# Kernel optimization log

Measured on AMD Instinct MI355X. Metric: run time of the kernel, lower is better.

Reference implementation:

```python
import jax, jax.numpy as jnp
import numpy as np


def _closest_dist_sum(p1, p2):
    # p1: [B, N, 3], p2: [B, M, 3]
    # Euclidean distance via the expanded quadratic form; matches
    # torch.norm(p1 - p2, 2, dim=3) -> min over p2 -> sum over all.
    d2 = (jnp.sum(p1 * p1, axis=-1)[:, :, None]
          + jnp.sum(p2 * p2, axis=-1)[:, None, :]
          - 2.0 * jnp.einsum('bnd,bmd->bnm', p1, p2))  # [B, N, M]
    d = jnp.sqrt(jnp.maximum(d2, 0.0))
    return jnp.sum(jnp.min(d, axis=2))


def setup_inputs() -> dict:
    key = jax.random.key(0)
    k1, k2 = jax.random.split(key)
    shape_xyz = jax.random.normal(k1, (8, 8192, 6), dtype=jnp.float32)
    skel_xyz = jax.random.normal(k2, (8, 2048, 3), dtype=jnp.float32)
    return {"shape_xyz": shape_xyz, "skel_xyz": skel_xyz}


def reference(shape_xyz, skel_xyz):
    # normals (shape_xyz[:, :, 3:6]) are extracted but unused in the loss
    pts = shape_xyz[:, :, :3]
    cd1 = _closest_dist_sum(pts, skel_xyz)   # shape -> skeleton
    cd2 = _closest_dist_sum(skel_xyz, pts)   # skeleton -> shape
    loss_cd = (cd1 + cd2) * 0.0001
    return loss_cd
```

## Files before the change

kernel.cpp:

```cpp
#include <hip/hip_runtime.h>

#define BATCH   8
#define SHAPE_N 8192
#define SKEL_M  2048
#define CHUNK   1024

#define WS2_OFF 512

typedef short bf16x8 __attribute__((ext_vector_type(8)));
typedef float f32x16 __attribute__((ext_vector_type(16)));
union FragU { bf16x8 v; uint4 u4; };

__device__ __forceinline__ unsigned int f2bf(float a) {
    unsigned int u = __float_as_uint(a);
    return (u + 0x7FFFu + ((u >> 16) & 1u)) >> 16;
}
__device__ __forceinline__ float bf2f(unsigned int h) {
    return __uint_as_float(h << 16);
}
__device__ __forceinline__ unsigned int pack2(unsigned int lo, unsigned int hi) {
    return lo | (hi << 16);
}
__device__ __forceinline__ void bfsplit(float v, unsigned int& h, unsigned int& l) {
    h = f2bf(v);
    l = f2bf(v - bf2f(h));
}

template <int SA, int SB>
__device__ __forceinline__ float cd_scan(
    const float* __restrict__ Araw,
    const float* __restrict__ Braw,
    uint4* sB, float* p_ra)
{
    const int tid = threadIdx.x;
    const int l = tid & 63;

    const float* p = Araw + (size_t)(l & 31) * SA;
    const float x = p[0], y = p[1], z = p[2];
    *p_ra = x * x + y * y + z * z;
    unsigned int hx, lx, hy, ly, hz, lz;
    bfsplit(x, hx, lx); bfsplit(y, hy, ly); bfsplit(z, hz, lz);
    const unsigned int one = 0x3F80u;
    FragU bf;
    if (l < 32) {
        bf.u4 = make_uint4(pack2(hx, hy), pack2(hz, one),
                           pack2(lx, ly), pack2(lz, one));
    } else {
        bf.u4 = make_uint4(pack2(hx, hy), pack2(hz, 0u), 0u, 0u);
    }

    const f32x16 Z = {0,0,0,0,0,0,0,0,0,0,0,0,0,0,0,0};
    float rmin = 3.4e38f;
    const unsigned int off0 = (unsigned int)((l >> 5) * 512 + (l & 31) * 16);

    for (int c = 0; c < 2048; c += CHUNK) {
        __syncthreads();
        const float* src = Braw + (size_t)c * SB;
        for (int i = tid; i < CHUNK; i += 256) {
            const float* q = src + (size_t)i * SB;
            const float bx = q[0], by = q[1], bz = q[2];
            const float cx = -2.f * bx, cy = -2.f * by, cz = -2.f * bz;
            const float rb = bx * bx + by * by + bz * bz;
            unsigned int chx, clx, chy, cly, chz, clz, rbh, rbl;
            bfsplit(cx, chx, clx); bfsplit(cy, chy, cly); bfsplit(cz, chz, clz);
            bfsplit(rb, rbh, rbl);
            const int g = i >> 5, r = i & 31;
            sB[g * 64 + r]      = make_uint4(pack2(chx, chy), pack2(chz, rbh),
                                             pack2(chx, chy), pack2(chz, rbl));
            sB[g * 64 + 32 + r] = make_uint4(pack2(clx, cly), pack2(clz, 0u),
                                             0u, 0u);
        }
        __syncthreads();

        unsigned int o = off0;
#pragma unroll 8
        for (int g = 0; g < CHUNK / 32; ++g) {
            FragU af;
            af.u4 = *(const uint4*)((const char*)sB + o);
            o += 1024;
            f32x16 D = __builtin_amdgcn_mfma_f32_32x32x16_bf16(af.v, bf.v, Z, 0, 0, 0);
            const float t0 = fminf(fminf(D[0],  D[1]),  D[2]);
            const float t1 = fminf(fminf(D[3],  D[4]),  D[5]);
            const float t2 = fminf(fminf(D[6],  D[7]),  D[8]);
            const float t3 = fminf(fminf(D[9],  D[10]), D[11]);
            const float t4 = fminf(fminf(D[12], D[13]), D[14]);
            const float u0 = fminf(fminf(t0, t1), t2);
            const float u1 = fminf(fminf(t3, t4), D[15]);
            rmin = fminf(rmin, fminf(u0, u1));
        }
    }
    rmin = fminf(rmin, __shfl_xor(rmin, 32, 64));
    return rmin;
}

__global__ __launch_bounds__(256) void cd_main(
    const float* __restrict__ shape, const float* __restrict__ skel,
    float* __restrict__ ws)
{
    __shared__ uint4 sB[CHUNK * 2];
    __shared__ float s_wsum[4];
    const int tid = threadIdx.x;
    const int l = tid & 63, wv = tid >> 6;
    const int bid = blockIdx.x;

    if (bid < 512) {
        const int b = bid >> 6, sub = bid & 63;
        float ra;
        const float rmin = cd_scan<6, 3>(
            shape + ((size_t)b * SHAPE_N + sub * 128 + wv * 32) * 6,
            skel + (size_t)b * SKEL_M * 3, sB, &ra);
        float d = (l < 32) ? sqrtf(fmaxf(ra + rmin, 0.f)) : 0.f;
        for (int o = 32; o; o >>= 1) d += __shfl_down(d, o, 64);
        if (l == 0) s_wsum[wv] = d;
        __syncthreads();
        if (tid == 0)
            ws[bid] = s_wsum[0] + s_wsum[1] + s_wsum[2] + s_wsum[3];
    } else {
        const int j = bid - 512;
        const int b = j >> 6, rem = j & 63;
        const int asub = rem >> 2, bs = rem & 3;
        float ra;
        const float rmin = cd_scan<3, 6>(
            skel + ((size_t)b * SKEL_M + asub * 128 + wv * 32) * 3,
            shape + ((size_t)b * SHAPE_N + bs * 2048) * 6, sB, &ra);
        if (l < 32)
            ws[WS2_OFF + bs * (BATCH * SKEL_M) + b * SKEL_M +
               asub * 128 + wv * 32 + l] = ra + rmin;
    }
}

__global__ __launch_bounds__(1024) void cd_reduce(
    const float* __restrict__ ws, float* __restrict__ out)
{
    __shared__ float s_wsum[16];
    const int t = threadIdx.x;
    float s = 0.f;

    const float4* w4 = (const float4*)(ws + WS2_OFF);
#pragma unroll
    for (int r = 0; r < 4; ++r) {
        const int i4 = r * 1024 + t;
        float4 v0 = w4[i4];
        const float4 v1 = w4[4096 + i4];
        const float4 v2 = w4[8192 + i4];
        const float4 v3 = w4[12288 + i4];
        v0.x = fminf(fminf(v0.x, v1.x), fminf(v2.x, v3.x));
        v0.y = fminf(fminf(v0.y, v1.y), fminf(v2.y, v3.y));
        v0.z = fminf(fminf(v0.z, v1.z), fminf(v2.z, v3.z));
        v0.w = fminf(fminf(v0.w, v1.w), fminf(v2.w, v3.w));
        s += sqrtf(fmaxf(v0.x, 0.f)) + sqrtf(fmaxf(v0.y, 0.f)) +
             sqrtf(fmaxf(v0.z, 0.f)) + sqrtf(fmaxf(v0.w, 0.f));
    }
    if (t < 512) s += ws[t];

    for (int o = 32; o; o >>= 1) s += __shfl_down(s, o, 64);
    const int lane = t & 63, wave = t >> 6;
    if (lane == 0) s_wsum[wave] = s;
    __syncthreads();
    if (t == 0) {
        float tot = 0.f;
#pragma unroll
        for (int w = 0; w < 16; ++w) tot += s_wsum[w];
        out[0] = tot * 1e-4f;
    }
}

extern "C" void kernel_launch(void* const* d_in, const int* in_sizes, int n_in,
                              void* d_out, int out_size, void* d_ws, size_t ws_size,
                              hipStream_t stream) {
    const float* shape = (const float*)d_in[0];
    const float* skel  = (const float*)d_in[1];
    float* out         = (float*)d_out;
    float* ws          = (float*)d_ws;

    cd_main<<<1024, 256, 0, stream>>>(shape, skel, ws);
    cd_reduce<<<1, 1024, 0, stream>>>(ws, out);
}
```

Measured before the change: 75.73 us.

## Process two 32-point A tiles per wave to reuse each LDS B fragment

Each wave now builds two B fragments (64 query points) and issues two MFMAs for every LDS-loaded A fragment, which halves LDS reads and the B-staging work per query point. The grid shrinks from 1024 to 512 blocks and the workspace layout and reduction offsets are adjusted to match. In exchange, register pressure goes up, the unroll factor is lowered, and fewer blocks are available to fill the 256 CUs.

Result: no change. 77.01 us (+1.7%).

```diff
diff --git a/kernel.cpp b/kernel.cpp
--- a/kernel.cpp
+++ b/kernel.cpp
@@ -5,7 +5,7 @@
 #define SKEL_M  2048
 #define CHUNK   1024
 
-#define WS2_OFF 512
+#define WS2_OFF 256
 
 typedef short bf16x8 __attribute__((ext_vector_type(8)));
 typedef float f32x16 __attribute__((ext_vector_type(16)));
@@ -26,31 +26,50 @@
     l = f2bf(v - bf2f(h));
 }
 
-template <int SA, int SB>
-__device__ __forceinline__ float cd_scan(
-    const float* __restrict__ Araw,
-    const float* __restrict__ Braw,
-    uint4* sB, float* p_ra)
+template <int SA>
+__device__ __forceinline__ void make_bfrag(
+    const float* __restrict__ ap, int l, FragU& bf, float& ra)
 {
-    const int tid = threadIdx.x;
-    const int l = tid & 63;
-
-    const float* p = Araw + (size_t)(l & 31) * SA;
-    const float x = p[0], y = p[1], z = p[2];
-    *p_ra = x * x + y * y + z * z;
+    const float x = ap[0], y = ap[1], z = ap[2];
+    ra = x * x + y * y + z * z;
     unsigned int hx, lx, hy, ly, hz, lz;
     bfsplit(x, hx, lx); bfsplit(y, hy, ly); bfsplit(z, hz, lz);
     const unsigned int one = 0x3F80u;
-    FragU bf;
     if (l < 32) {
         bf.u4 = make_uint4(pack2(hx, hy), pack2(hz, one),
                            pack2(lx, ly), pack2(lz, one));
     } else {
         bf.u4 = make_uint4(pack2(hx, hy), pack2(hz, 0u), 0u, 0u);
     }
+}
+
+__device__ __forceinline__ float min16(const f32x16& D) {
+    const float t0 = fminf(fminf(D[0],  D[1]),  D[2]);
+    const float t1 = fminf(fminf(D[3],  D[4]),  D[5]);
+    const float t2 = fminf(fminf(D[6],  D[7]),  D[8]);
+    const float t3 = fminf(fminf(D[9],  D[10]), D[11]);
+    const float t4 = fminf(fminf(D[12], D[13]), D[14]);
+    const float u0 = fminf(fminf(t0, t1), t2);
+    const float u1 = fminf(fminf(t3, t4), D[15]);
+    return fminf(u0, u1);
+}
+
+template <int SA, int SB>
+__device__ __forceinline__ void cd_scan2(
+    const float* __restrict__ Araw,
+    const float* __restrict__ Braw,
+    uint4* sB, float& rmin0o, float& rmin1o, float& ra0o, float& ra1o)
+{
+    const int tid = threadIdx.x;
+    const int l = tid & 63;
+
+    FragU bf0, bf1;
+    float ra0, ra1;
+    make_bfrag<SA>(Araw + (size_t)(l & 31) * SA, l, bf0, ra0);
+    make_bfrag<SA>(Araw + (size_t)(32 + (l & 31)) * SA, l, bf1, ra1);
 
     const f32x16 Z = {0,0,0,0,0,0,0,0,0,0,0,0,0,0,0,0};
-    float rmin = 3.4e38f;
+    float rmin0 = 3.4e38f, rmin1 = 3.4e38f;
     const unsigned int off0 = (unsigned int)((l >> 5) * 512 + (l & 31) * 16);
 
     for (int c = 0; c < 2048; c += CHUNK) {
@@ -73,24 +92,20 @@
         __syncthreads();
 
         unsigned int o = off0;
-#pragma unroll 8
+#pragma unroll 4
         for (int g = 0; g < CHUNK / 32; ++g) {
             FragU af;
             af.u4 = *(const uint4*)((const char*)sB + o);
             o += 1024;
-            f32x16 D = __builtin_amdgcn_mfma_f32_32x32x16_bf16(af.v, bf.v, Z, 0, 0, 0);
-            const float t0 = fminf(fminf(D[0],  D[1]),  D[2]);
-            const float t1 = fminf(fminf(D[3],  D[4]),  D[5]);
-            const float t2 = fminf(fminf(D[6],  D[7]),  D[8]);
-            const float t3 = fminf(fminf(D[9],  D[10]), D[11]);
-            const float t4 = fminf(fminf(D[12], D[13]), D[14]);
-            const float u0 = fminf(fminf(t0, t1), t2);
-            const float u1 = fminf(fminf(t3, t4), D[15]);
-            rmin = fminf(rmin, fminf(u0, u1));
+            f32x16 D0 = __builtin_amdgcn_mfma_f32_32x32x16_bf16(af.v, bf0.v, Z, 0, 0, 0);
+            f32x16 D1 = __builtin_amdgcn_mfma_f32_32x32x16_bf16(af.v, bf1.v, Z, 0, 0, 0);
+            rmin0 = fminf(rmin0, min16(D0));
+            rmin1 = fminf(rmin1, min16(D1));
         }
     }
-    rmin = fminf(rmin, __shfl_xor(rmin, 32, 64));
-    return rmin;
+    rmin0o = fminf(rmin0, __shfl_xor(rmin0, 32, 64));
+    rmin1o = fminf(rmin1, __shfl_xor(rmin1, 32, 64));
+    ra0o = ra0; ra1o = ra1;
 }
 
 __global__ __launch_bounds__(256) void cd_main(
@@ -103,29 +118,33 @@
     const int l = tid & 63, wv = tid >> 6;
     const int bid = blockIdx.x;
 
-    if (bid < 512) {
-        const int b = bid >> 6, sub = bid & 63;
-        float ra;
-        const float rmin = cd_scan<6, 3>(
-            shape + ((size_t)b * SHAPE_N + sub * 128 + wv * 32) * 6,
-            skel + (size_t)b * SKEL_M * 3, sB, &ra);
-        float d = (l < 32) ? sqrtf(fmaxf(ra + rmin, 0.f)) : 0.f;
+    if (bid < 256) {
+        const int b = bid >> 5, sub = bid & 31;
+        float rmin0, rmin1, ra0, ra1;
+        cd_scan2<6, 3>(shape + ((size_t)b * SHAPE_N + sub * 256 + wv * 64) * 6,
+                       skel + (size_t)b * SKEL_M * 3,
+                       sB, rmin0, rmin1, ra0, ra1);
+        float d = (l < 32) ? sqrtf(fmaxf(ra0 + rmin0, 0.f)) +
+                             sqrtf(fmaxf(ra1 + rmin1, 0.f)) : 0.f;
         for (int o = 32; o; o >>= 1) d += __shfl_down(d, o, 64);
         if (l == 0) s_wsum[wv] = d;
         __syncthreads();
         if (tid == 0)
             ws[bid] = s_wsum[0] + s_wsum[1] + s_wsum[2] + s_wsum[3];
     } else {
-        const int j = bid - 512;
-        const int b = j >> 6, rem = j & 63;
-        const int asub = rem >> 2, bs = rem & 3;
-        float ra;
-        const float rmin = cd_scan<3, 6>(
-            skel + ((size_t)b * SKEL_M + asub * 128 + wv * 32) * 3,
-            shape + ((size_t)b * SHAPE_N + bs * 2048) * 6, sB, &ra);
-        if (l < 32)
-            ws[WS2_OFF + bs * (BATCH * SKEL_M) + b * SKEL_M +
-               asub * 128 + wv * 32 + l] = ra + rmin;
+        const int j = bid - 256;
+        const int b = j >> 5, rem = j & 31;
+        const int asub = rem >> 2, q = rem & 3;
+        float rmin0, rmin1, ra0, ra1;
+        cd_scan2<3, 6>(skel + ((size_t)b * SKEL_M + asub * 256 + wv * 64) * 3,
+                       shape + ((size_t)b * SHAPE_N + q * 2048) * 6,
+                       sB, rmin0, rmin1, ra0, ra1);
+        if (l < 32) {
+            float* w = ws + WS2_OFF + q * (BATCH * SKEL_M) + b * SKEL_M +
+                       asub * 256 + wv * 64;
+            w[l]      = ra0 + rmin0;
+            w[32 + l] = ra1 + rmin1;
+        }
     }
 }
 
@@ -151,7 +170,7 @@
         s += sqrtf(fmaxf(v0.x, 0.f)) + sqrtf(fmaxf(v0.y, 0.f)) +
              sqrtf(fmaxf(v0.z, 0.f)) + sqrtf(fmaxf(v0.w, 0.f));
     }
-    if (t < 512) s += ws[t];
+    if (t < 256) s += ws[t];
 
     for (int o = 32; o; o >>= 1) s += __shfl_down(s, o, 64);
     const int lane = t & 63, wave = t >> 6;
@@ -173,6 +192,6 @@
     float* out         = (float*)d_out;
     float* ws          = (float*)d_ws;
 
-    cd_main<<<1024, 256, 0, stream>>>(shape, skel, ws);
+    cd_main<<<512, 256, 0, stream>>>(shape, skel, ws);
     cd_reduce<<<1, 1024, 0, stream>>>(ws, out);
 }
```

## Prepack operands into bf16 fragments in a separate kernel and stream from global

Applied to the files above, without the earlier changes.

Adds a pack kernel that converts every skeleton and shape point once into split-bf16 MFMA fragment layout in workspace. The main kernel then reads these fragments straight from global/L2 instead of having each block repack into LDS behind __syncthreads barriers. Blocks shrink to 128 threads, and each wave now handles two 32-row A tiles against the same stream. This removes redundant per-block conversion work and barriers, at the cost of an extra launch and global-memory fragment loads without LDS staging.

Result: slower. 96.58 us (+27.5%).

```diff
diff --git a/kernel.cpp b/kernel.cpp
--- a/kernel.cpp
+++ b/kernel.cpp
@@ -3,9 +3,7 @@
 #define BATCH   8
 #define SHAPE_N 8192
 #define SKEL_M  2048
-#define CHUNK   1024
-
-#define WS2_OFF 512
+
 
 typedef short bf16x8 __attribute__((ext_vector_type(8)));
 typedef float f32x16 __attribute__((ext_vector_type(16)));
@@ -26,79 +24,95 @@
     l = f2bf(v - bf2f(h));
 }
 
-template <int SA, int SB>
-__device__ __forceinline__ float cd_scan(
-    const float* __restrict__ Araw,
-    const float* __restrict__ Braw,
-    uint4* sB, float* p_ra)
-{
-    const int tid = threadIdx.x;
-    const int l = tid & 63;
-
-    const float* p = Araw + (size_t)(l & 31) * SA;
-    const float x = p[0], y = p[1], z = p[2];
-    *p_ra = x * x + y * y + z * z;
+__device__ __forceinline__ void make_bfrag(
+    const float* __restrict__ ap, int l, FragU& bf, float& ra)
+{
+    const float x = ap[0], y = ap[1], z = ap[2];
+    ra = x * x + y * y + z * z;
     unsigned int hx, lx, hy, ly, hz, lz;
     bfsplit(x, hx, lx); bfsplit(y, hy, ly); bfsplit(z, hz, lz);
     const unsigned int one = 0x3F80u;
-    FragU bf;
     if (l < 32) {
         bf.u4 = make_uint4(pack2(hx, hy), pack2(hz, one),
                            pack2(lx, ly), pack2(lz, one));
     } else {
         bf.u4 = make_uint4(pack2(hx, hy), pack2(hz, 0u), 0u, 0u);
     }
+}
+
+__device__ __forceinline__ float min16(const f32x16& D) {
+    const float t0 = fminf(fminf(D[0],  D[1]),  D[2]);
+    const float t1 = fminf(fminf(D[3],  D[4]),  D[5]);
+    const float t2 = fminf(fminf(D[6],  D[7]),  D[8]);
+    const float t3 = fminf(fminf(D[9],  D[10]), D[11]);
+    const float t4 = fminf(fminf(D[12], D[13]), D[14]);
+    const float u0 = fminf(fminf(t0, t1), t2);
+    const float u1 = fminf(fminf(t3, t4), D[15]);
+    return fminf(u0, u1);
+}
+
+__global__ __launch_bounds__(256) void cd_pack(
+    const float* __restrict__ shape, const float* __restrict__ skel,
+    uint4* __restrict__ skel_pk, uint4* __restrict__ shape_pk)
+{
+    const int bid = blockIdx.x, tid = threadIdx.x;
+    const float* q;
+    uint4* dst;
+    int g, r;
+    if (bid < 64) {
+        const int idx = bid * 256 + tid;
+        const int b = idx >> 11, i = idx & 2047;
+        q = skel + ((size_t)b * SKEL_M + i) * 3;
+        dst = skel_pk + (size_t)b * 4096;
+        g = i >> 5; r = i & 31;
+    } else {
+        const int idx = (bid - 64) * 256 + tid;
+        const int b = idx >> 13, i = idx & 8191;
+        q = shape + ((size_t)b * SHAPE_N + i) * 6;
+        dst = shape_pk + (size_t)b * 16384;
+        g = i >> 5; r = i & 31;
+    }
+    const float bx = q[0], by = q[1], bz = q[2];
+    const float cx = -2.f * bx, cy = -2.f * by, cz = -2.f * bz;
+    const float rb = bx * bx + by * by + bz * bz;
+    unsigned int chx, clx, chy, cly, chz, clz, rbh, rbl;
+    bfsplit(cx, chx, clx); bfsplit(cy, chy, cly); bfsplit(cz, chz, clz);
+    bfsplit(rb, rbh, rbl);
+    dst[g * 64 + r]      = make_uint4(pack2(chx, chy), pack2(chz, rbh),
+                                      pack2(chx, chy), pack2(chz, rbl));
+    dst[g * 64 + 32 + r] = make_uint4(pack2(clx, cly), pack2(clz, 0u), 0u, 0u);
+}
+
+template <int SA>
+__device__ __forceinline__ float cd_scan_g(
+    const float* __restrict__ Araw,
+    const uint4* __restrict__ pk,
+    float& ra_out)
+{
+    const int l = threadIdx.x & 63;
+    FragU bf;
+    make_bfrag(Araw + (size_t)(l & 31) * SA, l, bf, ra_out);
 
     const f32x16 Z = {0,0,0,0,0,0,0,0,0,0,0,0,0,0,0,0};
     float rmin = 3.4e38f;
-    const unsigned int off0 = (unsigned int)((l >> 5) * 512 + (l & 31) * 16);
-
-    for (int c = 0; c < 2048; c += CHUNK) {
-        __syncthreads();
-        const float* src = Braw + (size_t)c * SB;
-        for (int i = tid; i < CHUNK; i += 256) {
-            const float* q = src + (size_t)i * SB;
-            const float bx = q[0], by = q[1], bz = q[2];
-            const float cx = -2.f * bx, cy = -2.f * by, cz = -2.f * bz;
-            const float rb = bx * bx + by * by + bz * bz;
-            unsigned int chx, clx, chy, cly, chz, clz, rbh, rbl;
-            bfsplit(cx, chx, clx); bfsplit(cy, chy, cly); bfsplit(cz, chz, clz);
-            bfsplit(rb, rbh, rbl);
-            const int g = i >> 5, r = i & 31;
-            sB[g * 64 + r]      = make_uint4(pack2(chx, chy), pack2(chz, rbh),
-                                             pack2(chx, chy), pack2(chz, rbl));
-            sB[g * 64 + 32 + r] = make_uint4(pack2(clx, cly), pack2(clz, 0u),
-                                             0u, 0u);
-        }
-        __syncthreads();
-
-        unsigned int o = off0;
-#pragma unroll 8
-        for (int g = 0; g < CHUNK / 32; ++g) {
-            FragU af;
-            af.u4 = *(const uint4*)((const char*)sB + o);
-            o += 1024;
-            f32x16 D = __builtin_amdgcn_mfma_f32_32x32x16_bf16(af.v, bf.v, Z, 0, 0, 0);
-            const float t0 = fminf(fminf(D[0],  D[1]),  D[2]);
-            const float t1 = fminf(fminf(D[3],  D[4]),  D[5]);
-            const float t2 = fminf(fminf(D[6],  D[7]),  D[8]);
-            const float t3 = fminf(fminf(D[9],  D[10]), D[11]);
-            const float t4 = fminf(fminf(D[12], D[13]), D[14]);
-            const float u0 = fminf(fminf(t0, t1), t2);
-            const float u1 = fminf(fminf(t3, t4), D[15]);
-            rmin = fminf(rmin, fminf(u0, u1));
-        }
-    }
-    rmin = fminf(rmin, __shfl_xor(rmin, 32, 64));
-    return rmin;
-}
-
-__global__ __launch_bounds__(256) void cd_main(
+    const uint4* p = pk + ((l >> 5) * 32 + (l & 31));
+
+#pragma unroll 4
+    for (int g = 0; g < 64; ++g) {
+        FragU af;
+        af.u4 = p[(size_t)g * 64];
+        f32x16 D = __builtin_amdgcn_mfma_f32_32x32x16_bf16(af.v, bf.v, Z, 0, 0, 0);
+        rmin = fminf(rmin, min16(D));
+    }
+    return fminf(rmin, __shfl_xor(rmin, 32, 64));
+}
+
+__global__ __launch_bounds__(128) void cd_main(
     const float* __restrict__ shape, const float* __restrict__ skel,
-    float* __restrict__ ws)
-{
-    __shared__ uint4 sB[CHUNK * 2];
-    __shared__ float s_wsum[4];
+    const uint4* __restrict__ skel_pk, const uint4* __restrict__ shape_pk,
+    float* __restrict__ part1, float* __restrict__ part2)
+{
+    __shared__ float s_wsum[2];
     const int tid = threadIdx.x;
     const int l = tid & 63, wv = tid >> 6;
     const int bid = blockIdx.x;
@@ -106,37 +120,49 @@
     if (bid < 512) {
         const int b = bid >> 6, sub = bid & 63;
         float ra;
-        const float rmin = cd_scan<6, 3>(
-            shape + ((size_t)b * SHAPE_N + sub * 128 + wv * 32) * 6,
-            skel + (size_t)b * SKEL_M * 3, sB, &ra);
-        float d = (l < 32) ? sqrtf(fmaxf(ra + rmin, 0.f)) : 0.f;
+        const float rmin = cd_scan_g<6>(
+            shape + ((size_t)b * SHAPE_N + sub * 128 + wv * 64 + 0) * 6,
+            skel_pk + (size_t)b * 4096, ra);
+        float ra2;
+        const float rmin2 = cd_scan_g<6>(
+            shape + ((size_t)b * SHAPE_N + sub * 128 + wv * 64 + 32) * 6,
+            skel_pk + (size_t)b * 4096, ra2);
+        float d = (l < 32) ? sqrtf(fmaxf(ra + rmin, 0.f)) +
+                             sqrtf(fmaxf(ra2 + rmin2, 0.f)) : 0.f;
         for (int o = 32; o; o >>= 1) d += __shfl_down(d, o, 64);
         if (l == 0) s_wsum[wv] = d;
         __syncthreads();
-        if (tid == 0)
-            ws[bid] = s_wsum[0] + s_wsum[1] + s_wsum[2] + s_wsum[3];
+        if (tid == 0) part1[bid] = s_wsum[0] + s_wsum[1];
     } else {
         const int j = bid - 512;
         const int b = j >> 6, rem = j & 63;
-        const int asub = rem >> 2, bs = rem & 3;
-        float ra;
-        const float rmin = cd_scan<3, 6>(
-            skel + ((size_t)b * SKEL_M + asub * 128 + wv * 32) * 3,
-            shape + ((size_t)b * SHAPE_N + bs * 2048) * 6, sB, &ra);
-        if (l < 32)
-            ws[WS2_OFF + bs * (BATCH * SKEL_M) + b * SKEL_M +
-               asub * 128 + wv * 32 + l] = ra + rmin;
+        const int ablk = rem >> 2, q = rem & 3;
+        const uint4* stream = shape_pk + (size_t)b * 16384 + (size_t)q * 4096;
+        float ra, ra2;
+        const float rmin = cd_scan_g<3>(
+            skel + ((size_t)b * SKEL_M + ablk * 128 + wv * 64 + 0) * 3,
+            stream, ra);
+        const float rmin2 = cd_scan_g<3>(
+            skel + ((size_t)b * SKEL_M + ablk * 128 + wv * 64 + 32) * 3,
+            stream, ra2);
+        if (l < 32) {
+            float* w = part2 + (size_t)q * (BATCH * SKEL_M) + b * SKEL_M +
+                       ablk * 128 + wv * 64;
+            w[l]      = ra + rmin;
+            w[32 + l] = ra2 + rmin2;
+        }
     }
 }
 
 __global__ __launch_bounds__(1024) void cd_reduce(
-    const float* __restrict__ ws, float* __restrict__ out)
+    const float* __restrict__ part1, const float* __restrict__ part2,
+    float* __restrict__ out)
 {
     __shared__ float s_wsum[16];
     const int t = threadIdx.x;
     float s = 0.f;
 
-    const float4* w4 = (const float4*)(ws + WS2_OFF);
+    const float4* w4 = (const float4*)part2;
 #pragma unroll
     for (int r = 0; r < 4; ++r) {
         const int i4 = r * 1024 + t;
@@ -151,7 +177,7 @@
         s += sqrtf(fmaxf(v0.x, 0.f)) + sqrtf(fmaxf(v0.y, 0.f)) +
              sqrtf(fmaxf(v0.z, 0.f)) + sqrtf(fmaxf(v0.w, 0.f));
     }
-    if (t < 512) s += ws[t];
+    if (t < 512) s += part1[t];
 
     for (int o = 32; o; o >>= 1) s += __shfl_down(s, o, 64);
     const int lane = t & 63, wave = t >> 6;
@@ -171,8 +197,14 @@
     const float* shape = (const float*)d_in[0];
     const float* skel  = (const float*)d_in[1];
     float* out         = (float*)d_out;
-    float* ws          = (float*)d_ws;
-
-    cd_main<<<1024, 256, 0, stream>>>(shape, skel, ws);
-    cd_reduce<<<1, 1024, 0, stream>>>(ws, out);
-}
+
+    uint4* skel_pk  = (uint4*)d_ws;
+    uint4* shape_pk = skel_pk + 32768;
+    float* part1    = (float*)(shape_pk + 131072);
+    float* part2    = part1 + 512;
+
+    cd_pack<<<320, 256, 0, stream>>>(shape, skel, skel_pk, shape_pk);
+    cd_main<<<1024, 128, 0, stream>>>(shape, skel, skel_pk, shape_pk,
+                                      part1, part2);
+    cd_reduce<<<1, 1024, 0, stream>>>(part1, part2, out);
+}
```
